# Kernel optimization log

Hardware: AMD Instinct MI355X
Metric: run time of the kernel (lower is better)

The kernel has to match this reference:

```python
import jax, jax.numpy as jnp
import numpy as np

N_NODES = 51 * 51 * 51  # 132651, from h,w,d = (51,51,51)
AVG_DEG = 64
N_EDGES = N_NODES * AVG_DEG  # 8489664 (even, required by view([2, E//2]))


def setup_inputs() -> dict:
    key = jax.random.key(0)
    k1, k2, k3, k4 = jax.random.split(key, 4)
    x = jax.random.normal(k1, (N_NODES, 1), dtype=jnp.float32)
    W = jax.random.normal(k2, (1, 2), dtype=jnp.float32)  # GCNConv weight (in=1, out=2)
    b = jax.random.normal(k3, (2,), dtype=jnp.float32)    # GCNConv bias
    edge_index = jax.random.randint(k4, (2, N_EDGES), 0, N_NODES, dtype=jnp.int64)
    return {"x": x, "W": W, "b": b, "edge_index": edge_index}


def reference(x, W, b, edge_index):
    N = x.shape[0]
    row, col = edge_index[0], edge_index[1]  # source -> target (PyG flow)

    loop = jnp.arange(N, dtype=edge_index.dtype)
    row_sl = jnp.concatenate([row, loop])
    col_sl = jnp.concatenate([col, loop])
    deg = jax.ops.segment_sum(jnp.ones_like(col_sl, dtype=x.dtype), col_sl, num_segments=N)
    dinv = jnp.where(deg > 0, jax.lax.rsqrt(jnp.maximum(deg, 1e-12)), 0.0)
    norm = dinv[row_sl] * dinv[col_sl]  # [E + N]

    xw = x @ W  # [N, 2]
    msg = norm[:, None] * xw[row_sl]  # gather + scale
    h = jax.ops.segment_sum(msg, col_sl, num_segments=N) + b  # scatter-add aggregate
    h = jax.nn.relu(h)  # [N, 2]

    # Per-edge: sum over channels of endpoint features, fold halves, sigmoid
    y = jnp.sum(h[row] + h[col], axis=-1)           # [E]
    y = jnp.mean(y.reshape(2, -1), axis=0)[:, None]  # [E//2, 1]
    return jax.nn.sigmoid(y)
```

## Files before the change

### kernel.cpp

```cpp
#include <hip/hip_runtime.h>
#include <hip/hip_bf16.h>
#include <math.h>

constexpr int N_NODES = 51 * 51 * 51;
constexpr int N_EDGES = N_NODES * 64;
constexpr int E_HALF  = N_EDGES / 2;
constexpr int NP      = (N_NODES + 255) & ~255;

constexpr int PART_S = 36864;
constexpr int NP_S   = 4;
constexpr int PART_D  = 73728;
constexpr int NP_D    = 2;
constexpr int WORDS_D = PART_D / 2;

constexpr int PART_O   = 73728;
constexpr int NPASS_O  = 2;
constexpr int SBF_LEN  = PART_O * NPASS_O;
constexpr int OUT_BLOCKS = 256;


__global__ __launch_bounds__(1024) void k_deg_part(const int4* __restrict__ col4,
                                                   unsigned* __restrict__ partial,
                                                   int Bp) {
    __shared__ unsigned cnt[WORDS_D];
    const int p = blockIdx.x / Bp;
    const int b = blockIdx.x % Bp;
    const int base = p * PART_D;
    for (int j = threadIdx.x; j < WORDS_D; j += 1024) cnt[j] = 0u;
    __syncthreads();
    const int n4 = N_EDGES / 4;
    const int stride = Bp * 1024;
    int i = b * 1024 + threadIdx.x;
    bool valid = i < n4;
    int4 c;
    if (valid) c = col4[i];
    while (valid) {
        const int inext = i + stride;
        const bool vnext = inext < n4;
        int4 cn;
        if (vnext) cn = col4[inext];
        unsigned j;
        j = (unsigned)(c.x - base);
        if (j < (unsigned)PART_D) atomicAdd(&cnt[j >> 1], 1u << ((j & 1) << 4));
        j = (unsigned)(c.y - base);
        if (j < (unsigned)PART_D) atomicAdd(&cnt[j >> 1], 1u << ((j & 1) << 4));
        j = (unsigned)(c.z - base);
        if (j < (unsigned)PART_D) atomicAdd(&cnt[j >> 1], 1u << ((j & 1) << 4));
        j = (unsigned)(c.w - base);
        if (j < (unsigned)PART_D) atomicAdd(&cnt[j >> 1], 1u << ((j & 1) << 4));
        c = cn; i = inext; valid = vnext;
    }
    __syncthreads();
    unsigned* dst = partial + (size_t)blockIdx.x * WORDS_D;
    for (int j = threadIdx.x; j < WORDS_D; j += 1024) dst[j] = cnt[j];
}

__global__ __launch_bounds__(256) void k_reduceA(const unsigned* __restrict__ partial,
                                                 const float* __restrict__ x,
                                                 int Bp,
                                                 float* __restrict__ dinv,
                                                 float* __restrict__ u) {
    int v = blockIdx.x * 256 + threadIdx.x;
    if (v >= N_NODES) return;
    const int p = (v >= PART_D) ? 1 : 0;
    const int j = v - p * PART_D;
    const int word = j >> 1;
    const int sh = (j & 1) << 4;
    const unsigned* src = partial + (size_t)(p * Bp) * WORDS_D + word;
    unsigned deg = 1;
#pragma unroll 8
    for (int b = 0; b < Bp; ++b) deg += (src[(size_t)b * WORDS_D] >> sh) & 0xFFFFu;
    float d = rsqrtf((float)deg);
    dinv[v] = d;
    u[v] = d * x[v];
}

__global__ __launch_bounds__(1024) void k_scat_part(const int4* __restrict__ row4,
                                                    const int4* __restrict__ col4,
                                                    const float* __restrict__ u,
                                                    float* __restrict__ partial,
                                                    int Bp) {
    __shared__ float acc[PART_S];
    const int p = blockIdx.x / Bp;
    const int b = blockIdx.x % Bp;
    const int base = p * PART_S;
    for (int j = threadIdx.x; j < PART_S; j += 1024) acc[j] = 0.f;
    __syncthreads();
    const int n4 = N_EDGES / 4;
    const int stride = Bp * 1024;
    int i = b * 1024 + threadIdx.x;
    bool valid = i < n4;
    int4 c, r;
    if (valid) { c = col4[i]; r = row4[i]; }
    while (valid) {
        const int inext = i + stride;
        const bool vnext = inext < n4;
        int4 cn, rn;
        if (vnext) { cn = col4[inext]; rn = row4[inext]; }
        unsigned j;
        j = (unsigned)(c.x - base);
        if (j < (unsigned)PART_S) atomicAdd(&acc[j], u[r.x]);
        j = (unsigned)(c.y - base);
        if (j < (unsigned)PART_S) atomicAdd(&acc[j], u[r.y]);
        j = (unsigned)(c.z - base);
        if (j < (unsigned)PART_S) atomicAdd(&acc[j], u[r.z]);
        j = (unsigned)(c.w - base);
        if (j < (unsigned)PART_S) atomicAdd(&acc[j], u[r.w]);
        c = cn; r = rn; i = inext; valid = vnext;
    }
    __syncthreads();
    float* dst = partial + (size_t)blockIdx.x * PART_S;
    for (int j = threadIdx.x; j < PART_S; j += 1024) dst[j] = acc[j];
}

__global__ __launch_bounds__(256) void k_reduceB(const float* __restrict__ partial,
                                                 const float* __restrict__ dinv,
                                                 const float* __restrict__ u,
                                                 const float* __restrict__ W,
                                                 const float* __restrict__ bb,
                                                 int Bp,
                                                 __hip_bfloat16* __restrict__ sbf) {
    int v = blockIdx.x * 256 + threadIdx.x;
    if (v >= N_NODES) return;
    const int p = (unsigned)v / (unsigned)PART_S;
    const int j = v - p * PART_S;
    const float* src = partial + (size_t)(p * Bp) * PART_S + j;
    float g = 0.f;
#pragma unroll 8
    for (int b = 0; b < Bp; ++b) g += src[(size_t)b * PART_S];
    float t = dinv[v] * (g + u[v]);
    float h0 = fmaxf(fmaf(t, W[0], bb[0]), 0.f);
    float h1 = fmaxf(fmaf(t, W[1], bb[1]), 0.f);
    sbf[v] = __float2bfloat16(h0 + h1);
}


__global__ __launch_bounds__(256) void k_init_deg(int* __restrict__ deg) {
    int i = blockIdx.x * 256 + threadIdx.x;
    if (i < N_NODES) deg[i] = 1;
}

__global__ __launch_bounds__(256) void k_deg(const int4* __restrict__ col4,
                                             int* __restrict__ deg) {
    int i = blockIdx.x * 256 + threadIdx.x;
    const int stride = gridDim.x * 256;
    const int n4 = N_EDGES / 4;
    for (; i < n4; i += stride) {
        int4 c = col4[i];
        atomicAdd(&deg[c.x], 1); atomicAdd(&deg[c.y], 1);
        atomicAdd(&deg[c.z], 1); atomicAdd(&deg[c.w], 1);
    }
}

__global__ __launch_bounds__(256) void k_dinv(const int* __restrict__ deg,
                                              const float* __restrict__ x,
                                              float* __restrict__ dinv,
                                              float* __restrict__ t) {
    int i = blockIdx.x * 256 + threadIdx.x;
    if (i >= N_NODES) return;
    float d = rsqrtf((float)deg[i]);
    dinv[i] = d;
    t[i] = d * d * x[i];
}

__global__ __launch_bounds__(256) void k_scatter(const int4* __restrict__ row4,
                                                 const int4* __restrict__ col4,
                                                 const float* __restrict__ x,
                                                 const float* __restrict__ dinv,
                                                 float* __restrict__ t) {
    int i = blockIdx.x * 256 + threadIdx.x;
    const int stride = gridDim.x * 256;
    const int n4 = N_EDGES / 4;
    for (; i < n4; i += stride) {
        int4 r = row4[i];
        int4 c = col4[i];
        atomicAdd(&t[c.x], dinv[r.x] * dinv[c.x] * x[r.x]);
        atomicAdd(&t[c.y], dinv[r.y] * dinv[c.y] * x[r.y]);
        atomicAdd(&t[c.z], dinv[r.z] * dinv[c.z] * x[r.z]);
        atomicAdd(&t[c.w], dinv[r.w] * dinv[c.w] * x[r.w]);
    }
}

__global__ __launch_bounds__(256) void k_node(const float* __restrict__ t,
                                              const float* __restrict__ W,
                                              const float* __restrict__ b,
                                              __hip_bfloat16* __restrict__ sbf) {
    int i = blockIdx.x * 256 + threadIdx.x;
    if (i >= N_NODES) return;
    float tv = t[i];
    float h0 = fmaxf(fmaf(tv, W[0], b[0]), 0.f);
    float h1 = fmaxf(fmaf(tv, W[1], b[1]), 0.f);
    sbf[i] = __float2bfloat16(h0 + h1);
}


__device__ __forceinline__ float bf2f(ushort u) {
    return __uint_as_float((unsigned)u << 16);
}

__global__ __launch_bounds__(1024) void k_out_pass(const int4* __restrict__ rowA4,
                                                   const int4* __restrict__ colA4,
                                                   const int4* __restrict__ rowB4,
                                                   const int4* __restrict__ colB4,
                                                   const ushort* __restrict__ sbf,
                                                   float4* __restrict__ out,
                                                   int base, int final_pass) {
    __shared__ ushort sl[PART_O];
    {
        const uint4* src = (const uint4*)(sbf + base);
        uint4* dst = (uint4*)sl;
        for (int j = threadIdx.x; j < PART_O / 8; j += 1024) dst[j] = src[j];
    }
    __syncthreads();
    const int n4 = E_HALF / 4;
    const int stride = gridDim.x * 1024;
#pragma unroll 2
    for (int i = blockIdx.x * 1024 + threadIdx.x; i < n4; i += stride) {
        int4 ra = rowA4[i], ca = colA4[i], rb = rowB4[i], cb = colB4[i];
        float c0 = 0.f, c1 = 0.f, c2 = 0.f, c3 = 0.f;
        unsigned j;
        j = (unsigned)(ra.x - base); if (j < (unsigned)PART_O) c0 += bf2f(sl[j]);
        j = (unsigned)(ca.x - base); if (j < (unsigned)PART_O) c0 += bf2f(sl[j]);
        j = (unsigned)(rb.x - base); if (j < (unsigned)PART_O) c0 += bf2f(sl[j]);
        j = (unsigned)(cb.x - base); if (j < (unsigned)PART_O) c0 += bf2f(sl[j]);
        j = (unsigned)(ra.y - base); if (j < (unsigned)PART_O) c1 += bf2f(sl[j]);
        j = (unsigned)(ca.y - base); if (j < (unsigned)PART_O) c1 += bf2f(sl[j]);
        j = (unsigned)(rb.y - base); if (j < (unsigned)PART_O) c1 += bf2f(sl[j]);
        j = (unsigned)(cb.y - base); if (j < (unsigned)PART_O) c1 += bf2f(sl[j]);
        j = (unsigned)(ra.z - base); if (j < (unsigned)PART_O) c2 += bf2f(sl[j]);
        j = (unsigned)(ca.z - base); if (j < (unsigned)PART_O) c2 += bf2f(sl[j]);
        j = (unsigned)(rb.z - base); if (j < (unsigned)PART_O) c2 += bf2f(sl[j]);
        j = (unsigned)(cb.z - base); if (j < (unsigned)PART_O) c2 += bf2f(sl[j]);
        j = (unsigned)(ra.w - base); if (j < (unsigned)PART_O) c3 += bf2f(sl[j]);
        j = (unsigned)(ca.w - base); if (j < (unsigned)PART_O) c3 += bf2f(sl[j]);
        j = (unsigned)(rb.w - base); if (j < (unsigned)PART_O) c3 += bf2f(sl[j]);
        j = (unsigned)(cb.w - base); if (j < (unsigned)PART_O) c3 += bf2f(sl[j]);
        float4 o;
        if (final_pass) {
            float4 prev = out[i];
            o.x = 1.f / (1.f + __expf(-0.5f * (prev.x + c0)));
            o.y = 1.f / (1.f + __expf(-0.5f * (prev.y + c1)));
            o.z = 1.f / (1.f + __expf(-0.5f * (prev.z + c2)));
            o.w = 1.f / (1.f + __expf(-0.5f * (prev.w + c3)));
        } else {
            o.x = c0; o.y = c1; o.z = c2; o.w = c3;
        }
        out[i] = o;
    }
}


extern "C" void kernel_launch(void* const* d_in, const int* in_sizes, int n_in,
                              void* d_out, int out_size, void* d_ws, size_t ws_size,
                              hipStream_t stream) {
    const float* x = (const float*)d_in[0];
    const float* W = (const float*)d_in[1];
    const float* b = (const float*)d_in[2];
    const int*   ei = (const int*)d_in[3];
    const int* row = ei;
    const int* col = ei + N_EDGES;
    float* out = (float*)d_out;

    char* ws = (char*)d_ws;
    float* dinv = (float*)(ws);
    float* u    = (float*)(ws + (size_t)NP * 4);
    __hip_bfloat16* sbf = (__hip_bfloat16*)(ws + (size_t)NP * 8);
    char* partialBase = ws + (size_t)NP * 8 + (size_t)SBF_LEN * 2;
    size_t head = (size_t)NP * 8 + (size_t)SBF_LEN * 2;
    size_t avail = (ws_size > head) ? ws_size - head : 0;

    int Bp_d = (int)(avail / ((size_t)NP_D * WORDS_D * 4));
    if (Bp_d > 128) Bp_d = 128;
    int Bp_s = (int)(avail / ((size_t)NP_S * PART_S * 4));
    if (Bp_s > 64) Bp_s = 64;

    const int nodeBlocks = (N_NODES + 255) / 256;
    const int edgeBlocks = 2048;

    if (Bp_s >= 2 && Bp_d >= 2) {
        unsigned* partU = (unsigned*)partialBase;
        float*    partF = (float*)partialBase;
        k_deg_part<<<NP_D * Bp_d, 1024, 0, stream>>>((const int4*)col, partU, Bp_d);
        k_reduceA<<<nodeBlocks, 256, 0, stream>>>(partU, x, Bp_d, dinv, u);
        k_scat_part<<<NP_S * Bp_s, 1024, 0, stream>>>((const int4*)row, (const int4*)col,
                                                      u, partF, Bp_s);
        k_reduceB<<<nodeBlocks, 256, 0, stream>>>(partF, dinv, u, W, b, Bp_s, sbf);
    } else {
        int* deg = (int*)partialBase;
        k_init_deg<<<nodeBlocks, 256, 0, stream>>>(deg);
        k_deg<<<edgeBlocks, 256, 0, stream>>>((const int4*)col, deg);
        k_dinv<<<nodeBlocks, 256, 0, stream>>>(deg, x, dinv, u);
        k_scatter<<<edgeBlocks, 256, 0, stream>>>((const int4*)row, (const int4*)col,
                                                  x, dinv, u);
        k_node<<<nodeBlocks, 256, 0, stream>>>(u, W, b, sbf);
    }

    k_out_pass<<<OUT_BLOCKS, 1024, 0, stream>>>(
        (const int4*)row, (const int4*)col,
        (const int4*)(row + E_HALF), (const int4*)(col + E_HALF),
        (const ushort*)sbf, (float4*)out, 0, 0);
    k_out_pass<<<OUT_BLOCKS, 1024, 0, stream>>>(
        (const int4*)row, (const int4*)col,
        (const int4*)(row + E_HALF), (const int4*)(col + E_HALF),
        (const ushort*)sbf, (float4*)out, PART_O, 1);
}
```

Before: 133.5 us.

## Pack degree counts to 8 bits and scatter in fp16 via ds_pk_add_f16

Degree counting now packs four 8-bit counters per LDS word, so the whole node range fits in one shared array and each block reads the column indices only once instead of once per partition. The scatter stage stores messages as fp16 and accumulates them into packed-half LDS words with ds_pk_add_f16, which halves partition count from four to two and halves the partial buffer traffic. Node features are also switched from bf16 to fp16. The risks are 8-bit per-block degree counters overflowing if a block sees more than 255 hits on one node, and fp16 accumulation losing precision.

New measurement: 134.2 us. No clear change (+0.5%).

```diff
diff --git a/kernel.cpp b/kernel.cpp
--- a/kernel.cpp
+++ b/kernel.cpp
@@ -7,85 +7,75 @@
 constexpr int E_HALF  = N_EDGES / 2;
 constexpr int NP      = (N_NODES + 255) & ~255;
 
-constexpr int PART_S = 36864;
-constexpr int NP_S   = 4;
-constexpr int PART_D  = 73728;
-constexpr int NP_D    = 2;
-constexpr int WORDS_D = PART_D / 2;
-
+constexpr int WORDS_D8 = 36864;
+constexpr int PART_S2 = 73728;
+constexpr int NP_S2   = 2;
 constexpr int PART_O   = 73728;
-constexpr int NPASS_O  = 2;
-constexpr int SBF_LEN  = PART_O * NPASS_O;
+constexpr int SH_LEN   = PART_O * 2;
 constexpr int OUT_BLOCKS = 256;
 
-
-__global__ __launch_bounds__(1024) void k_deg_part(const int4* __restrict__ col4,
-                                                   unsigned* __restrict__ partial,
-                                                   int Bp) {
-    __shared__ unsigned cnt[WORDS_D];
-    const int p = blockIdx.x / Bp;
-    const int b = blockIdx.x % Bp;
-    const int base = p * PART_D;
-    for (int j = threadIdx.x; j < WORDS_D; j += 1024) cnt[j] = 0u;
+__device__ __forceinline__ float h2f(ushort u) {
+    return (float)__builtin_bit_cast(_Float16, u);
+}
+__device__ __forceinline__ ushort f2h(float f) {
+    return __builtin_bit_cast(unsigned short, (_Float16)f);
+}
+
+
+__global__ __launch_bounds__(1024) void k_deg8(const int4* __restrict__ col4,
+                                               unsigned* __restrict__ partial,
+                                               int Bp) {
+    __shared__ unsigned cnt[WORDS_D8];
+    for (int j = threadIdx.x; j < WORDS_D8; j += 1024) cnt[j] = 0u;
     __syncthreads();
     const int n4 = N_EDGES / 4;
     const int stride = Bp * 1024;
-    int i = b * 1024 + threadIdx.x;
-    bool valid = i < n4;
-    int4 c;
-    if (valid) c = col4[i];
-    while (valid) {
-        const int inext = i + stride;
-        const bool vnext = inext < n4;
-        int4 cn;
-        if (vnext) cn = col4[inext];
-        unsigned j;
-        j = (unsigned)(c.x - base);
-        if (j < (unsigned)PART_D) atomicAdd(&cnt[j >> 1], 1u << ((j & 1) << 4));
-        j = (unsigned)(c.y - base);
-        if (j < (unsigned)PART_D) atomicAdd(&cnt[j >> 1], 1u << ((j & 1) << 4));
-        j = (unsigned)(c.z - base);
-        if (j < (unsigned)PART_D) atomicAdd(&cnt[j >> 1], 1u << ((j & 1) << 4));
-        j = (unsigned)(c.w - base);
-        if (j < (unsigned)PART_D) atomicAdd(&cnt[j >> 1], 1u << ((j & 1) << 4));
-        c = cn; i = inext; valid = vnext;
-    }
-    __syncthreads();
-    unsigned* dst = partial + (size_t)blockIdx.x * WORDS_D;
-    for (int j = threadIdx.x; j < WORDS_D; j += 1024) dst[j] = cnt[j];
+#pragma unroll 2
+    for (int i = blockIdx.x * 1024 + threadIdx.x; i < n4; i += stride) {
+        int4 c = col4[i];
+        atomicAdd(&cnt[(unsigned)c.x >> 2], 1u << (((unsigned)c.x & 3u) << 3));
+        atomicAdd(&cnt[(unsigned)c.y >> 2], 1u << (((unsigned)c.y & 3u) << 3));
+        atomicAdd(&cnt[(unsigned)c.z >> 2], 1u << (((unsigned)c.z & 3u) << 3));
+        atomicAdd(&cnt[(unsigned)c.w >> 2], 1u << (((unsigned)c.w & 3u) << 3));
+    }
+    __syncthreads();
+    uint4* dst = (uint4*)(partial + (size_t)blockIdx.x * WORDS_D8);
+    const uint4* src = (const uint4*)cnt;
+    for (int j = threadIdx.x; j < WORDS_D8 / 4; j += 1024) dst[j] = src[j];
 }
 
 __global__ __launch_bounds__(256) void k_reduceA(const unsigned* __restrict__ partial,
                                                  const float* __restrict__ x,
                                                  int Bp,
                                                  float* __restrict__ dinv,
-                                                 float* __restrict__ u) {
+                                                 float* __restrict__ uf,
+                                                 ushort* __restrict__ uh) {
     int v = blockIdx.x * 256 + threadIdx.x;
     if (v >= N_NODES) return;
-    const int p = (v >= PART_D) ? 1 : 0;
-    const int j = v - p * PART_D;
-    const int word = j >> 1;
-    const int sh = (j & 1) << 4;
-    const unsigned* src = partial + (size_t)(p * Bp) * WORDS_D + word;
+    const unsigned* src = partial + ((unsigned)v >> 2);
+    const int sh = ((unsigned)v & 3u) << 3;
     unsigned deg = 1;
 #pragma unroll 8
-    for (int b = 0; b < Bp; ++b) deg += (src[(size_t)b * WORDS_D] >> sh) & 0xFFFFu;
+    for (int b = 0; b < Bp; ++b) deg += (src[(size_t)b * WORDS_D8] >> sh) & 0xFFu;
     float d = rsqrtf((float)deg);
     dinv[v] = d;
-    u[v] = d * x[v];
-}
-
-__global__ __launch_bounds__(1024) void k_scat_part(const int4* __restrict__ row4,
-                                                    const int4* __restrict__ col4,
-                                                    const float* __restrict__ u,
-                                                    float* __restrict__ partial,
-                                                    int Bp) {
-    __shared__ float acc[PART_S];
+    float uu = d * x[v];
+    uf[v] = uu;
+    uh[v] = f2h(uu);
+}
+
+__global__ __launch_bounds__(1024) void k_scat2(const int4* __restrict__ row4,
+                                                const int4* __restrict__ col4,
+                                                const ushort* __restrict__ uh,
+                                                ushort* __restrict__ partialH,
+                                                int Bp) {
+    __shared__ unsigned acc[PART_S2 / 2];
     const int p = blockIdx.x / Bp;
     const int b = blockIdx.x % Bp;
-    const int base = p * PART_S;
-    for (int j = threadIdx.x; j < PART_S; j += 1024) acc[j] = 0.f;
-    __syncthreads();
+    const int base = p * PART_S2;
+    for (int j = threadIdx.x; j < PART_S2 / 2; j += 1024) acc[j] = 0u;
+    __syncthreads();
+    const unsigned accBase = (unsigned)(uintptr_t)(&acc[0]);
     const int n4 = N_EDGES / 4;
     const int stride = Bp * 1024;
     int i = b * 1024 + threadIdx.x;
@@ -98,40 +88,42 @@
         int4 cn, rn;
         if (vnext) { cn = col4[inext]; rn = row4[inext]; }
         unsigned j;
-        j = (unsigned)(c.x - base);
-        if (j < (unsigned)PART_S) atomicAdd(&acc[j], u[r.x]);
-        j = (unsigned)(c.y - base);
-        if (j < (unsigned)PART_S) atomicAdd(&acc[j], u[r.y]);
-        j = (unsigned)(c.z - base);
-        if (j < (unsigned)PART_S) atomicAdd(&acc[j], u[r.z]);
-        j = (unsigned)(c.w - base);
-        if (j < (unsigned)PART_S) atomicAdd(&acc[j], u[r.w]);
+#define SCAT1(CC, RR)                                                          \
+        j = (unsigned)(CC - base);                                             \
+        if (j < (unsigned)PART_S2) {                                           \
+            unsigned pk = (unsigned)uh[RR] << ((j & 1u) << 4);                 \
+            unsigned off = accBase + ((j >> 1) << 2);                          \
+            asm volatile("ds_pk_add_f16 %0, %1" :: "v"(off), "v"(pk) : "memory"); \
+        }
+        SCAT1(c.x, r.x) SCAT1(c.y, r.y) SCAT1(c.z, r.z) SCAT1(c.w, r.w)
+#undef SCAT1
         c = cn; r = rn; i = inext; valid = vnext;
     }
     __syncthreads();
-    float* dst = partial + (size_t)blockIdx.x * PART_S;
-    for (int j = threadIdx.x; j < PART_S; j += 1024) dst[j] = acc[j];
-}
-
-__global__ __launch_bounds__(256) void k_reduceB(const float* __restrict__ partial,
+    uint4* dst = (uint4*)(partialH + (size_t)blockIdx.x * PART_S2);
+    const uint4* src = (const uint4*)acc;
+    for (int j = threadIdx.x; j < PART_S2 / 8; j += 1024) dst[j] = src[j];
+}
+
+__global__ __launch_bounds__(256) void k_reduceB(const ushort* __restrict__ partialH,
                                                  const float* __restrict__ dinv,
-                                                 const float* __restrict__ u,
+                                                 const float* __restrict__ uf,
                                                  const float* __restrict__ W,
                                                  const float* __restrict__ bb,
                                                  int Bp,
-                                                 __hip_bfloat16* __restrict__ sbf) {
+                                                 ushort* __restrict__ sh) {
     int v = blockIdx.x * 256 + threadIdx.x;
     if (v >= N_NODES) return;
-    const int p = (unsigned)v / (unsigned)PART_S;
-    const int j = v - p * PART_S;
-    const float* src = partial + (size_t)(p * Bp) * PART_S + j;
+    const int p = (v >= PART_S2) ? 1 : 0;
+    const int j = v - p * PART_S2;
+    const ushort* src = partialH + (size_t)(p * Bp) * PART_S2 + j;
     float g = 0.f;
 #pragma unroll 8
-    for (int b = 0; b < Bp; ++b) g += src[(size_t)b * PART_S];
-    float t = dinv[v] * (g + u[v]);
+    for (int b = 0; b < Bp; ++b) g += h2f(src[(size_t)b * PART_S2]);
+    float t = dinv[v] * (g + uf[v]);
     float h0 = fmaxf(fmaf(t, W[0], bb[0]), 0.f);
     float h1 = fmaxf(fmaf(t, W[1], bb[1]), 0.f);
-    sbf[v] = __float2bfloat16(h0 + h1);
+    sh[v] = f2h(h0 + h1);
 }
 
 
@@ -184,30 +176,26 @@
 __global__ __launch_bounds__(256) void k_node(const float* __restrict__ t,
                                               const float* __restrict__ W,
                                               const float* __restrict__ b,
-                                              __hip_bfloat16* __restrict__ sbf) {
+                                              ushort* __restrict__ sh) {
     int i = blockIdx.x * 256 + threadIdx.x;
     if (i >= N_NODES) return;
     float tv = t[i];
     float h0 = fmaxf(fmaf(tv, W[0], b[0]), 0.f);
     float h1 = fmaxf(fmaf(tv, W[1], b[1]), 0.f);
-    sbf[i] = __float2bfloat16(h0 + h1);
-}
-
-
-__device__ __forceinline__ float bf2f(ushort u) {
-    return __uint_as_float((unsigned)u << 16);
-}
+    sh[i] = f2h(h0 + h1);
+}
+
 
 __global__ __launch_bounds__(1024) void k_out_pass(const int4* __restrict__ rowA4,
                                                    const int4* __restrict__ colA4,
                                                    const int4* __restrict__ rowB4,
                                                    const int4* __restrict__ colB4,
-                                                   const ushort* __restrict__ sbf,
+                                                   const ushort* __restrict__ sh,
                                                    float4* __restrict__ out,
                                                    int base, int final_pass) {
     __shared__ ushort sl[PART_O];
     {
-        const uint4* src = (const uint4*)(sbf + base);
+        const uint4* src = (const uint4*)(sh + base);
         uint4* dst = (uint4*)sl;
         for (int j = threadIdx.x; j < PART_O / 8; j += 1024) dst[j] = src[j];
     }
@@ -219,22 +207,22 @@
         int4 ra = rowA4[i], ca = colA4[i], rb = rowB4[i], cb = colB4[i];
         float c0 = 0.f, c1 = 0.f, c2 = 0.f, c3 = 0.f;
         unsigned j;
-        j = (unsigned)(ra.x - base); if (j < (unsigned)PART_O) c0 += bf2f(sl[j]);
-        j = (unsigned)(ca.x - base); if (j < (unsigned)PART_O) c0 += bf2f(sl[j]);
-        j = (unsigned)(rb.x - base); if (j < (unsigned)PART_O) c0 += bf2f(sl[j]);
-        j = (unsigned)(cb.x - base); if (j < (unsigned)PART_O) c0 += bf2f(sl[j]);
-        j = (unsigned)(ra.y - base); if (j < (unsigned)PART_O) c1 += bf2f(sl[j]);
-        j = (unsigned)(ca.y - base); if (j < (unsigned)PART_O) c1 += bf2f(sl[j]);
-        j = (unsigned)(rb.y - base); if (j < (unsigned)PART_O) c1 += bf2f(sl[j]);
-        j = (unsigned)(cb.y - base); if (j < (unsigned)PART_O) c1 += bf2f(sl[j]);
-        j = (unsigned)(ra.z - base); if (j < (unsigned)PART_O) c2 += bf2f(sl[j]);
-        j = (unsigned)(ca.z - base); if (j < (unsigned)PART_O) c2 += bf2f(sl[j]);
-        j = (unsigned)(rb.z - base); if (j < (unsigned)PART_O) c2 += bf2f(sl[j]);
-        j = (unsigned)(cb.z - base); if (j < (unsigned)PART_O) c2 += bf2f(sl[j]);
-        j = (unsigned)(ra.w - base); if (j < (unsigned)PART_O) c3 += bf2f(sl[j]);
-        j = (unsigned)(ca.w - base); if (j < (unsigned)PART_O) c3 += bf2f(sl[j]);
-        j = (unsigned)(rb.w - base); if (j < (unsigned)PART_O) c3 += bf2f(sl[j]);
-        j = (unsigned)(cb.w - base); if (j < (unsigned)PART_O) c3 += bf2f(sl[j]);
+        j = (unsigned)(ra.x - base); if (j < (unsigned)PART_O) c0 += h2f(sl[j]);
+        j = (unsigned)(ca.x - base); if (j < (unsigned)PART_O) c0 += h2f(sl[j]);
+        j = (unsigned)(rb.x - base); if (j < (unsigned)PART_O) c0 += h2f(sl[j]);
+        j = (unsigned)(cb.x - base); if (j < (unsigned)PART_O) c0 += h2f(sl[j]);
+        j = (unsigned)(ra.y - base); if (j < (unsigned)PART_O) c1 += h2f(sl[j]);
+        j = (unsigned)(ca.y - base); if (j < (unsigned)PART_O) c1 += h2f(sl[j]);
+        j = (unsigned)(rb.y - base); if (j < (unsigned)PART_O) c1 += h2f(sl[j]);
+        j = (unsigned)(cb.y - base); if (j < (unsigned)PART_O) c1 += h2f(sl[j]);
+        j = (unsigned)(ra.z - base); if (j < (unsigned)PART_O) c2 += h2f(sl[j]);
+        j = (unsigned)(ca.z - base); if (j < (unsigned)PART_O) c2 += h2f(sl[j]);
+        j = (unsigned)(rb.z - base); if (j < (unsigned)PART_O) c2 += h2f(sl[j]);
+        j = (unsigned)(cb.z - base); if (j < (unsigned)PART_O) c2 += h2f(sl[j]);
+        j = (unsigned)(ra.w - base); if (j < (unsigned)PART_O) c3 += h2f(sl[j]);
+        j = (unsigned)(ca.w - base); if (j < (unsigned)PART_O) c3 += h2f(sl[j]);
+        j = (unsigned)(rb.w - base); if (j < (unsigned)PART_O) c3 += h2f(sl[j]);
+        j = (unsigned)(cb.w - base); if (j < (unsigned)PART_O) c3 += h2f(sl[j]);
         float4 o;
         if (final_pass) {
             float4 prev = out[i];
@@ -262,45 +250,46 @@
     float* out = (float*)d_out;
 
     char* ws = (char*)d_ws;
-    float* dinv = (float*)(ws);
-    float* u    = (float*)(ws + (size_t)NP * 4);
-    __hip_bfloat16* sbf = (__hip_bfloat16*)(ws + (size_t)NP * 8);
-    char* partialBase = ws + (size_t)NP * 8 + (size_t)SBF_LEN * 2;
-    size_t head = (size_t)NP * 8 + (size_t)SBF_LEN * 2;
+    float*  dinv = (float*)(ws);
+    float*  uf   = (float*)(ws + (size_t)NP * 4);
+    ushort* uh   = (ushort*)(ws + (size_t)NP * 8);
+    ushort* sh   = (ushort*)(ws + (size_t)NP * 10);
+    char* partialBase = ws + (size_t)NP * 10 + (size_t)SH_LEN * 2;
+    size_t head = (size_t)NP * 10 + (size_t)SH_LEN * 2;
     size_t avail = (ws_size > head) ? ws_size - head : 0;
 
-    int Bp_d = (int)(avail / ((size_t)NP_D * WORDS_D * 4));
+    int Bp_d = (int)(avail / 147456);
     if (Bp_d > 128) Bp_d = 128;
-    int Bp_s = (int)(avail / ((size_t)NP_S * PART_S * 4));
-    if (Bp_s > 64) Bp_s = 64;
+    int Bp_s = (int)(avail / (2 * 147456));
+    if (Bp_s > 128) Bp_s = 128;
 
     const int nodeBlocks = (N_NODES + 255) / 256;
     const int edgeBlocks = 2048;
 
     if (Bp_s >= 2 && Bp_d >= 2) {
         unsigned* partU = (unsigned*)partialBase;
-        float*    partF = (float*)partialBase;
-        k_deg_part<<<NP_D * Bp_d, 1024, 0, stream>>>((const int4*)col, partU, Bp_d);
-        k_reduceA<<<nodeBlocks, 256, 0, stream>>>(partU, x, Bp_d, dinv, u);
-        k_scat_part<<<NP_S * Bp_s, 1024, 0, stream>>>((const int4*)row, (const int4*)col,
-                                                      u, partF, Bp_s);
-        k_reduceB<<<nodeBlocks, 256, 0, stream>>>(partF, dinv, u, W, b, Bp_s, sbf);
+        ushort*   partH = (ushort*)partialBase;
+        k_deg8<<<Bp_d, 1024, 0, stream>>>((const int4*)col, partU, Bp_d);
+        k_reduceA<<<nodeBlocks, 256, 0, stream>>>(partU, x, Bp_d, dinv, uf, uh);
+        k_scat2<<<NP_S2 * Bp_s, 1024, 0, stream>>>((const int4*)row, (const int4*)col,
+                                                   uh, partH, Bp_s);
+        k_reduceB<<<nodeBlocks, 256, 0, stream>>>(partH, dinv, uf, W, b, Bp_s, sh);
     } else {
         int* deg = (int*)partialBase;
         k_init_deg<<<nodeBlocks, 256, 0, stream>>>(deg);
         k_deg<<<edgeBlocks, 256, 0, stream>>>((const int4*)col, deg);
-        k_dinv<<<nodeBlocks, 256, 0, stream>>>(deg, x, dinv, u);
+        k_dinv<<<nodeBlocks, 256, 0, stream>>>(deg, x, dinv, uf);
         k_scatter<<<edgeBlocks, 256, 0, stream>>>((const int4*)row, (const int4*)col,
-                                                  x, dinv, u);
-        k_node<<<nodeBlocks, 256, 0, stream>>>(u, W, b, sbf);
+                                                  x, dinv, uf);
+        k_node<<<nodeBlocks, 256, 0, stream>>>(uf, W, b, sh);
     }
 
     k_out_pass<<<OUT_BLOCKS, 1024, 0, stream>>>(
         (const int4*)row, (const int4*)col,
         (const int4*)(row + E_HALF), (const int4*)(col + E_HALF),
-        (const ushort*)sbf, (float4*)out, 0, 0);
+        sh, (float4*)out, 0, 0);
     k_out_pass<<<OUT_BLOCKS, 1024, 0, stream>>>(
         (const int4*)row, (const int4*)col,
         (const int4*)(row + E_HALF), (const int4*)(col + E_HALF),
-        (const ushort*)sbf, (float4*)out, PART_O, 1);
-}
+        sh, (float4*)out, PART_O, 1);
+}
```
